# Performance work log

Measured on AMD Instinct MI355X. Metric: run time of the kernel, lower is better.

Reference implementation:

```python
import jax, jax.numpy as jnp
import numpy as np


def setup_inputs() -> dict:
    key = jax.random.key(0)
    kx, kw = jax.random.split(key)
    B, S, IN, OUT = 4, 2048, 4096, 4096
    x = jax.random.normal(kx, (B, S, IN), dtype=jnp.float32)
    # int8-stored weight (kept as int32 container holding int8-range values)
    weight = jax.random.randint(kw, (IN, OUT), -127, 128, dtype=jnp.int32).astype(jnp.int8)
    return {"x": x, "weight": weight}


def reference(x, weight):
    # Faithful to: torch.matmul(x, self.weight.float())
    # inline dequant (int8 -> fp32) fused into the GEMM input
    w = weight.astype(jnp.float32)  # [IN, OUT]
    return jnp.einsum('bsi,io->bso', x, w)
```

## Files before the change

### kernel.cpp

```cpp
#include <hip/hip_runtime.h>
#include <hip/hip_bf16.h>

#define M_DIM 8192
#define N_DIM 4096
#define K_DIM 4096

typedef __attribute__((ext_vector_type(4))) int int4v;
typedef __attribute__((ext_vector_type(8))) short short8;
typedef __attribute__((ext_vector_type(4))) float floatx4;

__device__ __forceinline__ unsigned short f2bf(float f) {
    union { float f; unsigned int u; } cv; cv.f = f;
    unsigned int u = cv.u;
    return (unsigned short)((u + 0x7fffu + ((u >> 16) & 1u)) >> 16);
}

__global__ __launch_bounds__(256) void xq_kernel(const float* __restrict__ X,
                                                 char* __restrict__ Xq,
                                                 float* __restrict__ scales) {
    const int row = blockIdx.x;
    const int t = threadIdx.x;
    const float4* src = (const float4*)(X + (size_t)row * K_DIM);
    float4 v[4];
    float am = 0.f;
#pragma unroll
    for (int i = 0; i < 4; ++i) {
        v[i] = src[t + i * 256];
        am = fmaxf(am, fmaxf(fmaxf(fabsf(v[i].x), fabsf(v[i].y)),
                             fmaxf(fabsf(v[i].z), fabsf(v[i].w))));
    }
#pragma unroll
    for (int off = 32; off; off >>= 1) am = fmaxf(am, __shfl_xor(am, off, 64));
    __shared__ float wmax[4];
    if ((t & 63) == 0) wmax[t >> 6] = am;
    __syncthreads();
    am = fmaxf(fmaxf(wmax[0], wmax[1]), fmaxf(wmax[2], wmax[3]));
    am = fmaxf(am, 1e-20f);
    const float inv = 127.f / am;
    unsigned int* dst = (unsigned int*)(Xq + (size_t)row * K_DIM);
#pragma unroll
    for (int i = 0; i < 4; ++i) {
        int q0 = __float2int_rn(v[i].x * inv);
        int q1 = __float2int_rn(v[i].y * inv);
        int q2 = __float2int_rn(v[i].z * inv);
        int q3 = __float2int_rn(v[i].w * inv);
        dst[t + i * 256] = (unsigned int)(q0 & 255) | ((unsigned int)(q1 & 255) << 8) |
                           ((unsigned int)(q2 & 255) << 16) | ((unsigned int)q3 << 24);
    }
    if (t == 0) scales[row] = am * (1.f / 127.f);
}

__global__ __launch_bounds__(256) void wq_kernel(const int* __restrict__ W,
                                                 char* __restrict__ WT) {
    __shared__ int trans[64][17];
    const int t  = threadIdx.x;
    const int tn = blockIdx.x;
    const int tk = blockIdx.y;
    const int n  = t & 63;
    const int kg = t >> 6;

#pragma unroll
    for (int p = 0; p < 4; ++p) {
        const int kb = p * 16 + kg * 4;
        const int* src = W + (size_t)(tk * 64 + kb) * N_DIM + tn * 64 + n;
        int v0 = src[0];
        int v1 = src[N_DIM];
        int v2 = src[2 * N_DIM];
        int v3 = src[3 * N_DIM];
        trans[n][kb >> 2] = (v0 & 255) | ((v1 & 255) << 8) | ((v2 & 255) << 16) |
                            ((unsigned int)v3 << 24);
    }
    __syncthreads();

    const int n2 = t >> 2;
    const int c  = t & 3;
    int o0 = trans[n2][c * 4 + 0];
    int o1 = trans[n2][c * 4 + 1];
    int o2 = trans[n2][c * 4 + 2];
    int o3 = trans[n2][c * 4 + 3];
    char* dst = WT + (size_t)(tn * 64 + n2) * K_DIM + tk * 64 + c * 16;
    int4 o; o.x = o0; o.y = o1; o.z = o2; o.w = o3;
    *(int4*)dst = o;
}

__global__ __launch_bounds__(256) void gemm_i8(const char* __restrict__ A,
                                               const char* __restrict__ BT,
                                               const float* __restrict__ scales,
                                               float* __restrict__ C) {
    __shared__ __attribute__((aligned(16))) char sA[128 * 64];
    __shared__ __attribute__((aligned(16))) char sB[128 * 64];

    const int t    = threadIdx.x;
    const int lane = t & 63;
    const int wave = t >> 6;
    const int bn   = blockIdx.x;
    const int bm   = blockIdx.y;
    const int waveM = (wave >> 1) * 64;
    const int waveN = (wave & 1) * 64;

    const int sr = t >> 2;
    const int sc = (t & 3) << 4;
    const char* gA0 = A + (size_t)(bm * 128 + sr) * K_DIM + sc;
    const char* gA1 = gA0 + (size_t)64 * K_DIM;
    const char* gB0 = BT + (size_t)(bn * 128 + sr) * K_DIM + sc;
    const char* gB1 = gB0 + (size_t)64 * K_DIM;
    char* lA0 = sA + wave * 1024;
    char* lA1 = sA + 4096 + wave * 1024;
    char* lB0 = sB + wave * 1024;
    char* lB1 = sB + 4096 + wave * 1024;

    const int fr = lane & 15;
    const int fk = (lane >> 4) << 4;
    const char* fA = sA + (waveM + fr) * 64 + fk;
    const char* fB = sB + (waveN + fr) * 64 + fk;

    int4v acc[4][4];
#pragma unroll
    for (int i = 0; i < 4; ++i)
#pragma unroll
        for (int j = 0; j < 4; ++j) acc[i][j] = (int4v){0, 0, 0, 0};

    for (int k0 = 0; k0 < K_DIM; k0 += 64) {
        __builtin_amdgcn_global_load_lds((const __attribute__((address_space(1))) void*)gA0,
                                         (__attribute__((address_space(3))) void*)lA0, 16, 0, 0);
        __builtin_amdgcn_global_load_lds((const __attribute__((address_space(1))) void*)gA1,
                                         (__attribute__((address_space(3))) void*)lA1, 16, 0, 0);
        __builtin_amdgcn_global_load_lds((const __attribute__((address_space(1))) void*)gB0,
                                         (__attribute__((address_space(3))) void*)lB0, 16, 0, 0);
        __builtin_amdgcn_global_load_lds((const __attribute__((address_space(1))) void*)gB1,
                                         (__attribute__((address_space(3))) void*)lB1, 16, 0, 0);
        gA0 += 64; gA1 += 64; gB0 += 64; gB1 += 64;
        __syncthreads();

        int4v a[4], b[4];
#pragma unroll
        for (int i = 0; i < 4; ++i) a[i] = *(const int4v*)(fA + i * 16 * 64);
#pragma unroll
        for (int j = 0; j < 4; ++j) b[j] = *(const int4v*)(fB + j * 16 * 64);
#pragma unroll
        for (int i = 0; i < 4; ++i)
#pragma unroll
            for (int j = 0; j < 4; ++j)
                acc[i][j] = __builtin_amdgcn_mfma_i32_16x16x64_i8(a[i], b[j], acc[i][j], 0, 0, 0);
        __syncthreads();
    }

    const int er = (lane >> 4) << 2;
    const int ec = lane & 15;
#pragma unroll
    for (int i = 0; i < 4; ++i) {
        const size_t row0 = (size_t)(bm * 128 + waveM + i * 16 + er);
        const float4 s4 = *(const float4*)(scales + row0);
        const float sc4[4] = {s4.x, s4.y, s4.z, s4.w};
#pragma unroll
        for (int j = 0; j < 4; ++j) {
            const size_t col = (size_t)(bn * 128 + waveN + j * 16 + ec);
#pragma unroll
            for (int rr = 0; rr < 4; ++rr) {
                C[(row0 + rr) * N_DIM + col] = (float)acc[i][j][rr] * sc4[rr];
            }
        }
    }
}

__global__ __launch_bounds__(256) void gemm_fb(const float* __restrict__ X,
                                               const int* __restrict__ W,
                                               float* __restrict__ C) {
    __shared__ __attribute__((aligned(16))) unsigned short sA[128 * 32];
    __shared__ __attribute__((aligned(16))) unsigned short sB[128 * 32];

    const int t    = threadIdx.x;
    const int lane = t & 63;
    const int wave = t >> 6;
    const int bn   = blockIdx.x;
    const int bm   = blockIdx.y;
    const int waveM = (wave >> 1) * 64;
    const int waveN = (wave & 1) * 64;

    const int ar = t >> 1, ac = (t & 1) << 4;
    const float* gX = X + (size_t)(bm * 128 + ar) * K_DIM + ac;
    const int br = t >> 3, bc = (t & 7) << 4;
    const int* gW = W + (size_t)br * N_DIM + bn * 128 + bc;

    const int fr = lane & 15;
    const int fk = (lane >> 4) << 3;
    const unsigned short* fA = sA + (waveM + fr) * 32 + fk;
    const unsigned short* fB = sB + (waveN + fr) * 32 + fk;

    floatx4 acc[4][4];
#pragma unroll
    for (int i = 0; i < 4; ++i)
#pragma unroll
        for (int j = 0; j < 4; ++j) acc[i][j] = (floatx4){0.f, 0.f, 0.f, 0.f};

    for (int k0 = 0; k0 < K_DIM; k0 += 32) {
        {
            const float4* p = (const float4*)gX;
            float4 v0 = p[0], v1 = p[1], v2 = p[2], v3 = p[3];
            uint4 o0, o1;
            o0.x = (unsigned int)f2bf(v0.x) | ((unsigned int)f2bf(v0.y) << 16);
            o0.y = (unsigned int)f2bf(v0.z) | ((unsigned int)f2bf(v0.w) << 16);
            o0.z = (unsigned int)f2bf(v1.x) | ((unsigned int)f2bf(v1.y) << 16);
            o0.w = (unsigned int)f2bf(v1.z) | ((unsigned int)f2bf(v1.w) << 16);
            o1.x = (unsigned int)f2bf(v2.x) | ((unsigned int)f2bf(v2.y) << 16);
            o1.y = (unsigned int)f2bf(v2.z) | ((unsigned int)f2bf(v2.w) << 16);
            o1.z = (unsigned int)f2bf(v3.x) | ((unsigned int)f2bf(v3.y) << 16);
            o1.w = (unsigned int)f2bf(v3.z) | ((unsigned int)f2bf(v3.w) << 16);
            uint4* d = (uint4*)&sA[ar * 32 + ac];
            d[0] = o0; d[1] = o1;
        }
        {
#pragma unroll
            for (int q = 0; q < 4; ++q) {
                int4 v = ((const int4*)gW)[q];
                sB[(bc + q * 4 + 0) * 32 + br] = f2bf((float)v.x);
                sB[(bc + q * 4 + 1) * 32 + br] = f2bf((float)v.y);
                sB[(bc + q * 4 + 2) * 32 + br] = f2bf((float)v.z);
                sB[(bc + q * 4 + 3) * 32 + br] = f2bf((float)v.w);
            }
        }
        gX += 32;
        gW += (size_t)32 * N_DIM;
        __syncthreads();

        short8 a[4], b[4];
#pragma unroll
        for (int i = 0; i < 4; ++i) a[i] = *(const short8*)(fA + i * 16 * 32);
#pragma unroll
        for (int j = 0; j < 4; ++j) b[j] = *(const short8*)(fB + j * 16 * 32);
#pragma unroll
        for (int i = 0; i < 4; ++i)
#pragma unroll
            for (int j = 0; j < 4; ++j)
                acc[i][j] = __builtin_amdgcn_mfma_f32_16x16x32_bf16(a[i], b[j], acc[i][j], 0, 0, 0);
        __syncthreads();
    }

    const int er = (lane >> 4) << 2;
    const int ec = lane & 15;
#pragma unroll
    for (int i = 0; i < 4; ++i)
#pragma unroll
        for (int j = 0; j < 4; ++j) {
            const size_t row0 = (size_t)(bm * 128 + waveM + i * 16 + er);
            const size_t col  = (size_t)(bn * 128 + waveN + j * 16 + ec);
#pragma unroll
            for (int rr = 0; rr < 4; ++rr) C[(row0 + rr) * N_DIM + col] = acc[i][j][rr];
        }
}

extern "C" void kernel_launch(void* const* d_in, const int* in_sizes, int n_in,
                              void* d_out, int out_size, void* d_ws, size_t ws_size,
                              hipStream_t stream) {
    const float* x = (const float*)d_in[0];
    const int*   w = (const int*)d_in[1];
    float* out = (float*)d_out;

    const size_t bytesXq = (size_t)M_DIM * K_DIM;
    const size_t bytesWT = (size_t)K_DIM * N_DIM;
    const size_t bytesSc = (size_t)M_DIM * sizeof(float);

    if (ws_size >= bytesXq + bytesWT + bytesSc) {
        char*  Xq = (char*)d_ws;
        char*  WT = (char*)d_ws + bytesXq;
        float* Sc = (float*)((char*)d_ws + bytesXq + bytesWT);
        xq_kernel<<<M_DIM, 256, 0, stream>>>(x, Xq, Sc);
        wq_kernel<<<dim3(N_DIM / 64, K_DIM / 64), 256, 0, stream>>>(w, WT);
        gemm_i8<<<dim3(N_DIM / 128, M_DIM / 128), 256, 0, stream>>>(Xq, WT, Sc, out);
    } else {
        gemm_fb<<<dim3(N_DIM / 128, M_DIM / 128), 256, 0, stream>>>(x, w, out);
    }
}
```

Baseline: 434.1 us.

## Rewrite int8 GEMM with 256x256 tiles, double-buffered swizzled LDS, and ping-pong schedule

The int8 GEMM moves from 128x128 tiles with 4 waves to 256x256 tiles with 8 waves. It uses K steps of 128, a 128KB double-buffered LDS with an XOR-swizzled layout to avoid bank conflicts, and a staged schedule that interleaves async global-to-LDS loads with MFMA quadrants behind barriers and s_setprio. The aim is to hide global memory latency, raise data reuse per tile, and keep the matrix cores busy. The larger tile leaves only 256 blocks and uses heavy LDS and registers, so occupancy and tail effects become a risk.

```diff
diff --git a/kernel.cpp b/kernel.cpp
--- a/kernel.cpp
+++ b/kernel.cpp
@@ -83,78 +83,167 @@
     *(int4*)dst = o;
 }
 
-__global__ __launch_bounds__(256) void gemm_i8(const char* __restrict__ A,
-                                               const char* __restrict__ BT,
-                                               const float* __restrict__ scales,
-                                               float* __restrict__ C) {
-    __shared__ __attribute__((aligned(16))) char sA[128 * 64];
-    __shared__ __attribute__((aligned(16))) char sB[128 * 64];
+#define GLL(src, dst) __builtin_amdgcn_global_load_lds( \
+    (const __attribute__((address_space(1))) void*)(src), \
+    (__attribute__((address_space(3))) void*)(dst), 16, 0, 0)
+
+__global__ __launch_bounds__(512, 2) void gemm_i8(const char* __restrict__ A,
+                                                  const char* __restrict__ BT,
+                                                  const float* __restrict__ scales,
+                                                  float* __restrict__ C) {
+    __shared__ __attribute__((aligned(16))) char lds[131072];
 
     const int t    = threadIdx.x;
     const int lane = t & 63;
     const int wave = t >> 6;
     const int bn   = blockIdx.x;
     const int bm   = blockIdx.y;
-    const int waveM = (wave >> 1) * 64;
-    const int waveN = (wave & 1) * 64;
-
-    const int sr = t >> 2;
-    const int sc = (t & 3) << 4;
-    const char* gA0 = A + (size_t)(bm * 128 + sr) * K_DIM + sc;
-    const char* gA1 = gA0 + (size_t)64 * K_DIM;
-    const char* gB0 = BT + (size_t)(bn * 128 + sr) * K_DIM + sc;
-    const char* gB1 = gB0 + (size_t)64 * K_DIM;
-    char* lA0 = sA + wave * 1024;
-    char* lA1 = sA + 4096 + wave * 1024;
-    char* lB0 = sB + wave * 1024;
-    char* lB1 = sB + 4096 + wave * 1024;
-
-    const int fr = lane & 15;
-    const int fk = (lane >> 4) << 4;
-    const char* fA = sA + (waveM + fr) * 64 + fk;
-    const char* fB = sB + (waveN + fr) * 64 + fk;
-
-    int4v acc[4][4];
-#pragma unroll
-    for (int i = 0; i < 4; ++i)
+    const int waveM = (wave >> 2) * 128;
+    const int waveN = (wave & 3) * 64;
+
+    const int srow = t >> 3;
+    const int schk = (t & 7) ^ (srow & 7);
+    const char* aSrc = A  + (size_t)(bm * 256 + srow) * K_DIM + schk * 16;
+    const char* bSrc = BT + (size_t)(bn * 256 + srow) * K_DIM + schk * 16;
+    char* aDst = lds + wave * 1024;
+    char* bDst = lds + 65536 + wave * 1024;
+
+#define STG_A(buf, r0, kt) do { \
+    GLL(aSrc + (size_t)(r0) * K_DIM + (kt) * 128,        aDst + (buf) * 32768 + (r0) * 128); \
+    GLL(aSrc + (size_t)((r0) + 64) * K_DIM + (kt) * 128, aDst + (buf) * 32768 + ((r0) + 64) * 128); \
+} while (0)
+#define STG_B(buf, r0, kt) do { \
+    GLL(bSrc + (size_t)(r0) * K_DIM + (kt) * 128,        bDst + (buf) * 32768 + (r0) * 128); \
+    GLL(bSrc + (size_t)((r0) + 64) * K_DIM + (kt) * 128, bDst + (buf) * 32768 + ((r0) + 64) * 128); \
+} while (0)
+
+    const char* fA = lds + (waveM + (lane & 15)) * 128;
+    const char* fB = lds + 65536 + (waveN + (lane & 15)) * 128;
+    const int sw0 = (((lane >> 4) + 0) ^ (lane & 7)) * 16;
+    const int sw1 = (((lane >> 4) + 4) ^ (lane & 7)) * 16;
+
+    int4v acc[8][4];
+#pragma unroll
+    for (int i = 0; i < 8; ++i)
 #pragma unroll
         for (int j = 0; j < 4; ++j) acc[i][j] = (int4v){0, 0, 0, 0};
 
-    for (int k0 = 0; k0 < K_DIM; k0 += 64) {
-        __builtin_amdgcn_global_load_lds((const __attribute__((address_space(1))) void*)gA0,
-                                         (__attribute__((address_space(3))) void*)lA0, 16, 0, 0);
-        __builtin_amdgcn_global_load_lds((const __attribute__((address_space(1))) void*)gA1,
-                                         (__attribute__((address_space(3))) void*)lA1, 16, 0, 0);
-        __builtin_amdgcn_global_load_lds((const __attribute__((address_space(1))) void*)gB0,
-                                         (__attribute__((address_space(3))) void*)lB0, 16, 0, 0);
-        __builtin_amdgcn_global_load_lds((const __attribute__((address_space(1))) void*)gB1,
-                                         (__attribute__((address_space(3))) void*)lB1, 16, 0, 0);
-        gA0 += 64; gA1 += 64; gB0 += 64; gB1 += 64;
-        __syncthreads();
-
-        int4v a[4], b[4];
-#pragma unroll
-        for (int i = 0; i < 4; ++i) a[i] = *(const int4v*)(fA + i * 16 * 64);
-#pragma unroll
-        for (int j = 0; j < 4; ++j) b[j] = *(const int4v*)(fB + j * 16 * 64);
-#pragma unroll
-        for (int i = 0; i < 4; ++i)
-#pragma unroll
-            for (int j = 0; j < 4; ++j)
-                acc[i][j] = __builtin_amdgcn_mfma_i32_16x16x64_i8(a[i], b[j], acc[i][j], 0, 0, 0);
-        __syncthreads();
+    int4v a[4][2], b[4][2];
+
+#define LDA(buf, mh) do { \
+    _Pragma("unroll") \
+    for (int i2 = 0; i2 < 4; ++i2) { \
+        a[i2][0] = *(const int4v*)(fA + (buf) * 32768 + ((mh) * 4 + i2) * 2048 + sw0); \
+        a[i2][1] = *(const int4v*)(fA + (buf) * 32768 + ((mh) * 4 + i2) * 2048 + sw1); \
+    } \
+} while (0)
+#define LDB(buf, j0) do { \
+    _Pragma("unroll") \
+    for (int j2 = 0; j2 < 2; ++j2) { \
+        b[(j0) + j2][0] = *(const int4v*)(fB + (buf) * 32768 + ((j0) + j2) * 2048 + sw0); \
+        b[(j0) + j2][1] = *(const int4v*)(fB + (buf) * 32768 + ((j0) + j2) * 2048 + sw1); \
+    } \
+} while (0)
+#define MFMAQ(mh, j0) do { \
+    _Pragma("unroll") \
+    for (int i2 = 0; i2 < 4; ++i2) \
+    _Pragma("unroll") \
+    for (int j2 = 0; j2 < 2; ++j2) { \
+        acc[(mh) * 4 + i2][(j0) + j2] = __builtin_amdgcn_mfma_i32_16x16x64_i8( \
+            a[i2][0], b[(j0) + j2][0], acc[(mh) * 4 + i2][(j0) + j2], 0, 0, 0); \
+        acc[(mh) * 4 + i2][(j0) + j2] = __builtin_amdgcn_mfma_i32_16x16x64_i8( \
+            a[i2][1], b[(j0) + j2][1], acc[(mh) * 4 + i2][(j0) + j2], 0, 0, 0); \
+    } \
+} while (0)
+
+    STG_A(0, 0, 0); STG_A(0, 128, 0);
+    STG_B(0, 0, 0); STG_B(0, 128, 0);
+    STG_B(1, 0, 1); STG_B(1, 128, 1);
+
+#pragma unroll 1
+    for (int it = 0; it < 16; ++it) {
+        const int kt = it * 2;
+        const bool more = (it < 15);
+
+        STG_A(1, 0, kt + 1);
+        asm volatile("s_waitcnt vmcnt(6)" ::: "memory");
+        __builtin_amdgcn_s_barrier();
+        LDA(0, 0); LDB(0, 0);
+        __builtin_amdgcn_s_setprio(1);
+        MFMAQ(0, 0);
+        __builtin_amdgcn_s_setprio(0);
+        __builtin_amdgcn_s_barrier();
+
+        STG_A(1, 128, kt + 1);
+        LDB(0, 2);
+        __builtin_amdgcn_s_barrier();
+        __builtin_amdgcn_s_setprio(1);
+        MFMAQ(0, 2);
+        __builtin_amdgcn_s_setprio(0);
+        __builtin_amdgcn_s_barrier();
+
+        if (more) STG_B(0, 0, kt + 2);
+        LDA(0, 1);
+        __builtin_amdgcn_s_barrier();
+        __builtin_amdgcn_s_setprio(1);
+        MFMAQ(1, 2);
+        __builtin_amdgcn_s_setprio(0);
+        __builtin_amdgcn_s_barrier();
+
+        if (more) STG_B(0, 128, kt + 2);
+        __builtin_amdgcn_s_barrier();
+        __builtin_amdgcn_s_setprio(1);
+        MFMAQ(1, 0);
+        __builtin_amdgcn_s_setprio(0);
+        __builtin_amdgcn_s_barrier();
+
+        if (more) {
+            STG_A(0, 0, kt + 2);
+            asm volatile("s_waitcnt vmcnt(6)" ::: "memory");
+        } else {
+            asm volatile("s_waitcnt vmcnt(0)" ::: "memory");
+        }
+        __builtin_amdgcn_s_barrier();
+        LDA(1, 0); LDB(1, 0);
+        __builtin_amdgcn_s_setprio(1);
+        MFMAQ(0, 0);
+        __builtin_amdgcn_s_setprio(0);
+        __builtin_amdgcn_s_barrier();
+
+        if (more) STG_A(0, 128, kt + 2);
+        LDB(1, 2);
+        __builtin_amdgcn_s_barrier();
+        __builtin_amdgcn_s_setprio(1);
+        MFMAQ(0, 2);
+        __builtin_amdgcn_s_setprio(0);
+        __builtin_amdgcn_s_barrier();
+
+        if (more) STG_B(1, 0, kt + 3);
+        LDA(1, 1);
+        __builtin_amdgcn_s_barrier();
+        __builtin_amdgcn_s_setprio(1);
+        MFMAQ(1, 2);
+        __builtin_amdgcn_s_setprio(0);
+        __builtin_amdgcn_s_barrier();
+
+        if (more) STG_B(1, 128, kt + 3);
+        __builtin_amdgcn_s_barrier();
+        __builtin_amdgcn_s_setprio(1);
+        MFMAQ(1, 0);
+        __builtin_amdgcn_s_setprio(0);
+        __builtin_amdgcn_s_barrier();
     }
 
     const int er = (lane >> 4) << 2;
     const int ec = lane & 15;
 #pragma unroll
-    for (int i = 0; i < 4; ++i) {
-        const size_t row0 = (size_t)(bm * 128 + waveM + i * 16 + er);
+    for (int i = 0; i < 8; ++i) {
+        const size_t row0 = (size_t)(bm * 256 + waveM + i * 16 + er);
         const float4 s4 = *(const float4*)(scales + row0);
         const float sc4[4] = {s4.x, s4.y, s4.z, s4.w};
 #pragma unroll
         for (int j = 0; j < 4; ++j) {
-            const size_t col = (size_t)(bn * 128 + waveN + j * 16 + ec);
+            const size_t col = (size_t)(bn * 256 + waveN + j * 16 + ec);
 #pragma unroll
             for (int rr = 0; rr < 4; ++rr) {
                 C[(row0 + rr) * N_DIM + col] = (float)acc[i][j][rr] * sc4[rr];
@@ -266,7 +355,7 @@
         float* Sc = (float*)((char*)d_ws + bytesXq + bytesWT);
         xq_kernel<<<M_DIM, 256, 0, stream>>>(x, Xq, Sc);
         wq_kernel<<<dim3(N_DIM / 64, K_DIM / 64), 256, 0, stream>>>(w, WT);
-        gemm_i8<<<dim3(N_DIM / 128, M_DIM / 128), 256, 0, stream>>>(Xq, WT, Sc, out);
+        gemm_i8<<<dim3(N_DIM / 256, M_DIM / 256), 512, 0, stream>>>(Xq, WT, Sc, out);
     } else {
         gemm_fb<<<dim3(N_DIM / 128, M_DIM / 128), 256, 0, stream>>>(x, w, out);
     }
```

Measured after the change: 383.5 us. -11.7%, faster.
